# Kernel tuning notes

Hardware: AMD Instinct MI355X
Metric: run time of the kernel (lower is better)

Reference implementation:

```python
import jax, jax.numpy as jnp
import numpy as np

V, E, H, L = 32000, 512, 512, 2   # vocab, emb_dim, hidden_dim, lstm layers
IN = 2 * H                        # input_size (= enc_output feature dim)
B, S_ENC, T_DEC = 32, 128, 64


def setup_inputs() -> dict:
    key = jax.random.key(0)
    ks = jax.random.split(key, 20)
    sc = 0.05
    inp = {
        "tokens": jax.random.randint(ks[0], (B, T_DEC), 0, V),
        "enc_output": jax.random.normal(ks[1], (B, S_ENC, IN), jnp.float32),
        "enc_h": jax.random.normal(ks[2], (L, B, H), jnp.float32),
        "enc_c": jax.random.normal(ks[3], (L, B, H), jnp.float32),
        "emb": jax.random.normal(ks[4], (V, E), jnp.float32) * sc,
        # attention MLP: attn1 in = H*L + IN, out = 4H; attn2: 4H -> 1
        "attn1_w": jax.random.normal(ks[5], (4 * H, H * L + IN), jnp.float32) * sc,
        "attn1_b": jnp.zeros((4 * H,), jnp.float32),
        "attn2_w": jax.random.normal(ks[6], (1, 4 * H), jnp.float32) * sc,
        "attn2_b": jnp.zeros((1,), jnp.float32),
        # LSTM layer 0: input E + IN; layer 1: input H. PyTorch gate order i,f,g,o
        "w_ih0": jax.random.normal(ks[7], (4 * H, E + IN), jnp.float32) * sc,
        "w_hh0": jax.random.normal(ks[8], (4 * H, H), jnp.float32) * sc,
        "b_ih0": jnp.zeros((4 * H,), jnp.float32),
        "b_hh0": jnp.zeros((4 * H,), jnp.float32),
        "w_ih1": jax.random.normal(ks[9], (4 * H, H), jnp.float32) * sc,
        "w_hh1": jax.random.normal(ks[10], (4 * H, H), jnp.float32) * sc,
        "b_ih1": jnp.zeros((4 * H,), jnp.float32),
        "b_hh1": jnp.zeros((4 * H,), jnp.float32),
        "out_w": jax.random.normal(ks[11], (V, H), jnp.float32) * sc,
        "out_b": jnp.zeros((V,), jnp.float32),
    }
    return inp


def _lstm_cell(x, h, c, w_ih, w_hh, b_ih, b_hh):
    g = x @ w_ih.T + h @ w_hh.T + (b_ih + b_hh)
    i, f, gg, o = jnp.split(g, 4, axis=-1)
    c_new = jax.nn.sigmoid(f) * c + jax.nn.sigmoid(i) * jnp.tanh(gg)
    h_new = jax.nn.sigmoid(o) * jnp.tanh(c_new)
    return h_new, c_new


def reference(tokens, enc_output, enc_h, enc_c, emb,
              attn1_w, attn1_b, attn2_w, attn2_b,
              w_ih0, w_hh0, b_ih0, b_hh0,
              w_ih1, w_hh1, b_ih1, b_hh1,
              out_w, out_b):
    b, s_enc = enc_output.shape[0], enc_output.shape[1]

    def context(h):  # h: [L, B, H] -> context: [B, 2H]
        hflat = jnp.transpose(h, (1, 0, 2)).reshape(b, -1)          # [B, L*H]
        hexp = jnp.broadcast_to(hflat[:, None, :], (b, s_enc, hflat.shape[-1]))
        ai = jnp.concatenate([enc_output, hexp], axis=-1)           # [B, S, 2H+L*H]
        hid = ai @ attn1_w.T + attn1_b                               # [B, S, 4H]
        logits = hid @ attn2_w.T + attn2_b                           # [B, S, 1]
        w = jax.nn.softmax(logits, axis=1)
        return jnp.sum(enc_output * w, axis=1)                       # [B, 2H]

    def step(carry, emb_t):  # emb_t: [B, E]
        h, c = carry
        ctx = context(h)
        x = jnp.concatenate([emb_t, ctx], axis=-1)                   # [B, E+2H]
        h0, c0 = _lstm_cell(x, h[0], c[0], w_ih0, w_hh0, b_ih0, b_hh0)
        h1, c1 = _lstm_cell(h0, h[1], c[1], w_ih1, w_hh1, b_ih1, b_hh1)
        return (jnp.stack([h0, h1]), jnp.stack([c0, c1])), h1

    emb_seq = jnp.transpose(emb[tokens], (1, 0, 2))                  # [T, B, E]
    _, outs = jax.lax.scan(step, (enc_h, enc_c), emb_seq)            # [T, B, H]
    dec = jnp.transpose(outs, (1, 0, 2))                             # [B, T, H]
    return dec @ out_w.T + out_b                                     # [B, T, V]
```

## Files before the change

kernel.cpp:

```cpp
#include <hip/hip_runtime.h>
#include <hip/hip_bf16.h>

typedef __attribute__((ext_vector_type(4))) float f4v;
typedef __attribute__((ext_vector_type(4))) short s4v;
typedef __attribute__((ext_vector_type(8))) short s8v;

#define DEVINL __device__ __forceinline__
#define NBLK 128
#define PADK 536
#define WROWS (16 * PADK)
#define HSLOT 16384

DEVINL short f2bf(float f) {
  unsigned u = __float_as_uint(f);
  u += 0x7FFFu + ((u >> 16) & 1u);
  return (short)(u >> 16);
}
DEVINL float bf2f(short s) {
  return __uint_as_float(((unsigned)(unsigned short)s) << 16);
}
DEVINL float sigm(float x) { return 1.f / (1.f + expf(-x)); }

DEVINL void cstore64(short* p, unsigned long long d) {
  asm volatile("global_store_dwordx2 %0, %1, off sc0 sc1"
               :: "v"(p), "v"(d) : "memory");
}

__global__ __launch_bounds__(256) void k_init2(const float* __restrict__ enc_h,
                                               short* __restrict__ hbuf,
                                               unsigned* __restrict__ arr) {
  int i = blockIdx.x * 256 + threadIdx.x;
  hbuf[i] = f2bf(enc_h[i]);
  hbuf[(long)65 * HSLOT + i] = f2bf(enc_h[16384 + i]);
  if (i < NBLK * 32 + 32) arr[i] = ((i & 31) == 16) ? 1u : 0u;
}

__global__ __launch_bounds__(256) void k_weff(const float* __restrict__ attn1_w,
                                              const float* __restrict__ attn2_w,
                                              float* __restrict__ w_enc) {
  __shared__ float part[8][32];
  int t = threadIdx.x;
  int jl = t & 31, kp = t >> 5;
  int j = blockIdx.x * 32 + jl;
  float acc = 0.f;
  for (int k = kp * 256; k < kp * 256 + 256; ++k)
    acc += attn2_w[k] * attn1_w[(long)k * 2048 + j];
  part[kp][jl] = acc;
  __syncthreads();
  if (t < 32) {
    float s = 0.f;
    for (int p = 0; p < 8; ++p) s += part[p][t];
    w_enc[blockIdx.x * 32 + t] = s;
  }
}

__global__ __launch_bounds__(256) void k_attn(const float* __restrict__ enc,
                                              const float* __restrict__ w_enc,
                                              float* __restrict__ ctx) {
  __shared__ float red[256];
  __shared__ float wls[128];
  int b = blockIdx.x, t = threadIdx.x;
  int s = t >> 1, half = t & 1;
  const float* e = enc + ((long)b * 128 + s) * 1024 + half * 512;
  const float* wv = w_enc + half * 512;
  float acc = 0.f;
  for (int k = 0; k < 512; k += 4) {
    f4v ev = *(const f4v*)(e + k);
    f4v w4 = *(const f4v*)(wv + k);
    acc += ev[0] * w4[0] + ev[1] * w4[1] + ev[2] * w4[2] + ev[3] * w4[3];
  }
  red[t] = acc;
  __syncthreads();
  if (half == 0) wls[s] = red[t] + red[t + 1];
  __syncthreads();
  red[t] = (t < 128) ? wls[t] : -3.4e38f;
  __syncthreads();
  for (int off = 128; off >= 1; off >>= 1) {
    if (t < off) red[t] = fmaxf(red[t], red[t + off]);
    __syncthreads();
  }
  float mx = red[0];
  __syncthreads();
  if (t < 128) { float ex = expf(wls[t] - mx); wls[t] = ex; red[t] = ex; }
  else red[t] = 0.f;
  __syncthreads();
  for (int off = 128; off >= 1; off >>= 1) {
    if (t < off) red[t] += red[t + off];
    __syncthreads();
  }
  float inv = 1.f / red[0];
  __syncthreads();
  if (t < 128) wls[t] *= inv;
  __syncthreads();
  float a0 = 0.f, a1 = 0.f, a2 = 0.f, a3 = 0.f;
  for (int ss = 0; ss < 128; ++ss) {
    float w = wls[ss];
    const float* er = enc + ((long)b * 128 + ss) * 1024;
    a0 += w * er[t];
    a1 += w * er[t + 256];
    a2 += w * er[t + 512];
    a3 += w * er[t + 768];
  }
  ctx[b * 1024 + t] = a0;
  ctx[b * 1024 + t + 256] = a1;
  ctx[b * 1024 + t + 512] = a2;
  ctx[b * 1024 + t + 768] = a3;
}

__global__ __launch_bounds__(256) void k_ctxpre(const float* __restrict__ w_ih0,
                                                const float* __restrict__ b_ih0,
                                                const float* __restrict__ b_hh0,
                                                const float* __restrict__ ctx,
                                                float* __restrict__ ctxpre) {
  int t = threadIdx.x;
  int j = blockIdx.x * 8 + (t >> 5);
  int b = t & 31;
  float acc = b_ih0[j] + b_hh0[j];
  const float* w = w_ih0 + (long)j * 1536 + 512;
  const float* c = ctx + b * 1024;
  for (int k = 0; k < 1024; k += 4) {
    f4v wv = *(const f4v*)(w + k);
    f4v cv = *(const f4v*)(c + k);
    acc += wv[0] * cv[0] + wv[1] * cv[1] + wv[2] * cv[2] + wv[3] * cv[3];
  }
  ctxpre[b * 2048 + j] = acc;
}

__global__ __launch_bounds__(256) void k_cvt(const float* __restrict__ src,
                                             short* __restrict__ dst) {
  long i = ((long)blockIdx.x * 256 + threadIdx.x) * 8;
  f4v a = *(const f4v*)(src + i);
  f4v b = *(const f4v*)(src + i + 4);
  s8v o;
  o[0] = f2bf(a[0]); o[1] = f2bf(a[1]); o[2] = f2bf(a[2]); o[3] = f2bf(a[3]);
  o[4] = f2bf(b[0]); o[5] = f2bf(b[1]); o[6] = f2bf(b[2]); o[7] = f2bf(b[3]);
  *(s8v*)(dst + i) = o;
}

template <int MODE>
__global__ __launch_bounds__(256) void gemm_bf16(
    const float* __restrict__ A, const float* __restrict__ B,
    const int* __restrict__ a_rows, const float* __restrict__ bias,
    float* __restrict__ C, int K, int lda, int ldb, int ldc) {
  __shared__ short As[128 * 72];
  __shared__ short Bs[128 * 72];
  int n0 = blockIdx.x * 128, m0 = blockIdx.y * 128;
  int t = threadIdx.x;
  int lane = t & 63, w = t >> 6;
  int wm = w & 1, wn = w >> 1;
  f4v acc[4][4];
#pragma unroll
  for (int mi = 0; mi < 4; ++mi)
#pragma unroll
    for (int ni = 0; ni < 4; ++ni) acc[mi][ni] = (f4v){0.f, 0.f, 0.f, 0.f};

  int sr = t >> 1;
  int sh = (t & 1) * 32;
  long arow = a_rows ? (long)a_rows[m0 + sr] : (long)(m0 + sr);
  const float* ap = A + arow * lda + sh;
  const float* bp = B + (long)(n0 + sr) * ldb + sh;
  short* as = &As[sr * 72 + sh];
  short* bs = &Bs[sr * 72 + sh];

  for (int k0 = 0; k0 < K; k0 += 64) {
#pragma unroll
    for (int i = 0; i < 8; ++i) {
      f4v va = *(const f4v*)(ap + k0 + i * 4);
      f4v vb = *(const f4v*)(bp + k0 + i * 4);
      s4v sa, sb;
      sa[0] = f2bf(va[0]); sa[1] = f2bf(va[1]); sa[2] = f2bf(va[2]); sa[3] = f2bf(va[3]);
      sb[0] = f2bf(vb[0]); sb[1] = f2bf(vb[1]); sb[2] = f2bf(vb[2]); sb[3] = f2bf(vb[3]);
      *(s4v*)(as + i * 4) = sa;
      *(s4v*)(bs + i * 4) = sb;
    }
    __syncthreads();
#pragma unroll
    for (int ks = 0; ks < 2; ++ks) {
      s8v af[4], bf[4];
#pragma unroll
      for (int mi = 0; mi < 4; ++mi)
        af[mi] = *(const s8v*)&As[(wm * 64 + mi * 16 + (lane & 15)) * 72 + ks * 32 + (lane >> 4) * 8];
#pragma unroll
      for (int ni = 0; ni < 4; ++ni)
        bf[ni] = *(const s8v*)&Bs[(wn * 64 + ni * 16 + (lane & 15)) * 72 + ks * 32 + (lane >> 4) * 8];
#pragma unroll
      for (int mi = 0; mi < 4; ++mi)
#pragma unroll
        for (int ni = 0; ni < 4; ++ni)
          acc[mi][ni] = __builtin_amdgcn_mfma_f32_16x16x32_bf16(af[mi], bf[ni], acc[mi][ni], 0, 0, 0);
    }
    __syncthreads();
  }
  int fq = lane >> 4, fr = lane & 15;
#pragma unroll
  for (int mi = 0; mi < 4; ++mi)
#pragma unroll
    for (int ni = 0; ni < 4; ++ni) {
      int col = n0 + wn * 64 + ni * 16 + fr;
      long rowb = m0 + wm * 64 + mi * 16 + fq * 4;
      if (MODE == 2) {
        int bz = (col & 511) >> 2;
        int c = ((col >> 9) << 2) + (col & 3);
#pragma unroll
        for (int r = 0; r < 4; ++r) {
          long m = rowb + r;
          C[(long)bz * 32768 + (m & 63) * 512 + (m >> 6) * 16 + c] = acc[mi][ni][r];
        }
      } else {
        float bv = bias ? bias[col] : 0.f;
#pragma unroll
        for (int r = 0; r < 4; ++r) C[(rowb + r) * (long)ldc + col] = acc[mi][ni][r] + bv;
      }
    }
}

template <bool BCVT>
__global__ __launch_bounds__(256) void gemm_out(
    const short* __restrict__ A, const short* __restrict__ Bbf,
    const float* __restrict__ Bf, const float* __restrict__ bias,
    float* __restrict__ C) {
  __shared__ short As[128 * 72];
  __shared__ short Bs[128 * 72];
  int m0 = blockIdx.x * 128, n0 = blockIdx.y * 128;
  int t = threadIdx.x;
  int lane = t & 63, w = t >> 6;
  int wm = w & 1, wn = w >> 1;
  f4v acc[4][4];
#pragma unroll
  for (int mi = 0; mi < 4; ++mi)
#pragma unroll
    for (int ni = 0; ni < 4; ++ni) acc[mi][ni] = (f4v){0.f, 0.f, 0.f, 0.f};

  int sr = t >> 1;
  int sh = (t & 1) * 32;
  const short* ap = A + (long)(m0 + sr) * 512 + sh;
  const short* bpb = Bbf + (long)(n0 + sr) * 512 + sh;
  const float* bpf = Bf + (long)(n0 + sr) * 512 + sh;
  short* as = &As[sr * 72 + sh];
  short* bs = &Bs[sr * 72 + sh];

  for (int k0 = 0; k0 < 512; k0 += 64) {
#pragma unroll
    for (int i = 0; i < 4; ++i)
      *(s8v*)(as + i * 8) = *(const s8v*)(ap + k0 + i * 8);
    if (BCVT) {
#pragma unroll
      for (int i = 0; i < 8; ++i) {
        f4v vb = *(const f4v*)(bpf + k0 + i * 4);
        s4v sb;
        sb[0] = f2bf(vb[0]); sb[1] = f2bf(vb[1]); sb[2] = f2bf(vb[2]); sb[3] = f2bf(vb[3]);
        *(s4v*)(bs + i * 4) = sb;
      }
    } else {
#pragma unroll
      for (int i = 0; i < 4; ++i)
        *(s8v*)(bs + i * 8) = *(const s8v*)(bpb + k0 + i * 8);
    }
    __syncthreads();
#pragma unroll
    for (int ks = 0; ks < 2; ++ks) {
      s8v af[4], bf[4];
#pragma unroll
      for (int mi = 0; mi < 4; ++mi)
        af[mi] = *(const s8v*)&As[(wm * 64 + mi * 16 + (lane & 15)) * 72 + ks * 32 + (lane >> 4) * 8];
#pragma unroll
      for (int ni = 0; ni < 4; ++ni)
        bf[ni] = *(const s8v*)&Bs[(wn * 64 + ni * 16 + (lane & 15)) * 72 + ks * 32 + (lane >> 4) * 8];
#pragma unroll
      for (int mi = 0; mi < 4; ++mi)
#pragma unroll
        for (int ni = 0; ni < 4; ++ni)
          acc[mi][ni] = __builtin_amdgcn_mfma_f32_16x16x32_bf16(af[mi], bf[ni], acc[mi][ni], 0, 0, 0);
    }
    __syncthreads();
  }
  int fq = lane >> 4, fr = lane & 15;
#pragma unroll
  for (int mi = 0; mi < 4; ++mi)
#pragma unroll
    for (int ni = 0; ni < 4; ++ni) {
      int col = n0 + wn * 64 + ni * 16 + fr;
      float bv = bias[col];
      long rowb = m0 + wm * 64 + mi * 16 + fq * 4;
#pragma unroll
      for (int r = 0; r < 4; ++r)
        __builtin_nontemporal_store(acc[mi][ni][r] + bv, &C[(rowb + r) * 32000L + col]);
    }
}

__global__ __launch_bounds__(256, 1) void lstm_persist(
    const float* __restrict__ w_hh0, const float* __restrict__ w_ih1,
    const float* __restrict__ w_hh1,
    const float* __restrict__ b_ih1, const float* __restrict__ b_hh1,
    const float* __restrict__ enc_c,
    const float* __restrict__ embp2, const float* __restrict__ ctxpre,
    short* __restrict__ hbuf, short* __restrict__ h1seqbf,
    unsigned* __restrict__ arr) {
  __shared__ alignas(16) short wlds[6 * WROWS];
  __shared__ float ctxp_l[32][16];
  __shared__ float bias1_l[16];
  __shared__ float gbuf[2][2][32][17];

  const int tid = threadIdx.x;
  const int hb4 = blockIdx.x * 4;
  const int lane = tid & 63, wid = tid >> 6;
  const int mt = wid & 1, kh = wid >> 1;
  const int fr = lane & 15, fq = lane >> 4;

  for (int base = tid * 4; base < 48 * 512; base += 1024) {
    int row = base >> 9, k = base & 511;
    int m = row >> 4, c = row & 15;
    int j = ((c >> 2) << 9) + hb4 + (c & 3);
    const float* wsrc = (m == 0) ? w_hh0 : ((m == 1) ? w_ih1 : w_hh1);
    f4v v = *(const f4v*)(wsrc + (long)j * 512 + k);
    short* hi = &wlds[(m * 2) * WROWS + c * PADK + k];
    short* lo = &wlds[(m * 2 + 1) * WROWS + c * PADK + k];
#pragma unroll
    for (int e = 0; e < 4; ++e) {
      short hh = f2bf(v[e]);
      hi[e] = hh;
      lo[e] = f2bf(v[e] - bf2f(hh));
    }
  }
  for (int i = tid; i < 512; i += 256) {
    int b = i >> 4, c = i & 15;
    ctxp_l[b][c] = ctxpre[b * 2048 + ((c >> 2) << 9) + hb4 + (c & 3)];
  }
  if (tid < 16) {
    int j = ((tid >> 2) << 9) + hb4 + (tid & 3);
    bias1_l[tid] = b_ih1[j] + b_hh1[j];
  }
  const int cq = (tid & 127) >> 2, cr = tid & 3;
  float c0r = 0.f, c1r = 0.f;
  if (tid < 128) c0r = enc_c[cq * 512 + hb4 + cr];
  else           c1r = enc_c[16384 + cq * 512 + hb4 + cr];
  __syncthreads();
  asm volatile("s_waitcnt vmcnt(0)" ::: "memory");
  asm volatile("buffer_inv sc1" ::: "memory");
  __syncthreads();

  short* H0 = hbuf;
  short* H1 = hbuf + (long)65 * HSLOT;
  const int foff = (mt * 16 + fr) * 512 + kh * 256 + fq * 8;
  const int woff = fr * PADK + kh * 256 + fq * 8;

  for (int p = 0; p <= 64; ++p) {
    const bool do_l0 = (p < 64), do_l1 = (p > 0);
    float e4[4] = {0.f, 0.f, 0.f, 0.f};
    if (do_l0 && tid < 128) {
      const float* ep = embp2 + (long)blockIdx.x * 32768 + p * 512 + cq * 16 + cr;
#pragma unroll
      for (int g = 0; g < 4; ++g) e4[g] = ep[g * 4];
    }
    if (p) {
      if (tid < NBLK)
        while (__hip_atomic_load(&arr[tid << 5], __ATOMIC_RELAXED,
                                 __HIP_MEMORY_SCOPE_AGENT) < (unsigned)p)
          __builtin_amdgcn_s_sleep(1);
      __syncthreads();
    }
    const short* a0 = H0 + (long)p * HSLOT + foff;
    s8v A0[8];
#pragma unroll
    for (int ks = 0; ks < 8; ++ks) A0[ks] = *(const s8v*)(a0 + ks * 32);
    if (do_l0) {
      f4v l0h = {0.f, 0.f, 0.f, 0.f}, l0l = l0h;
      const short* b0h = &wlds[0 * WROWS + woff];
      const short* b0l = &wlds[1 * WROWS + woff];
#pragma unroll
      for (int ks = 0; ks < 8; ++ks) {
        s8v B0h = *(const s8v*)(b0h + ks * 32);
        s8v B0l = *(const s8v*)(b0l + ks * 32);
        l0h = __builtin_amdgcn_mfma_f32_16x16x32_bf16(A0[ks], B0h, l0h, 0, 0, 0);
        l0l = __builtin_amdgcn_mfma_f32_16x16x32_bf16(A0[ks], B0l, l0l, 0, 0, 0);
      }
      f4v s = l0h + l0l;
#pragma unroll
      for (int r = 0; r < 4; ++r) gbuf[0][kh][mt * 16 + fq * 4 + r][fr] = s[r];
    }
    __syncthreads();
    if (do_l0) {
      if (tid < 128) {
        float g4[4];
#pragma unroll
        for (int g = 0; g < 4; ++g) {
          int c = g * 4 + cr;
          g4[g] = gbuf[0][0][cq][c] + gbuf[0][1][cq][c] + ctxp_l[cq][c] + e4[g];
        }
        float cn = sigm(g4[1]) * c0r + sigm(g4[0]) * tanhf(g4[2]);
        float hn = sigm(g4[3]) * tanhf(cn);
        c0r = cn;
        unsigned v16 = (unsigned)(unsigned short)f2bf(hn);
        unsigned p01 = v16 | ((unsigned)__shfl_down((int)v16, 1) << 16);
        unsigned long long wd = (unsigned long long)p01 |
            ((unsigned long long)(unsigned)__shfl_down((int)p01, 2) << 32);
        if ((tid & 3) == 0)
          cstore64(H0 + (long)(p + 1) * HSLOT + cq * 512 + hb4, wd);
      }
      asm volatile("s_waitcnt vmcnt(0)" ::: "memory");
      __syncthreads();
      if (tid == 0)
        __hip_atomic_store(&arr[(unsigned)blockIdx.x << 5], (unsigned)(p + 1),
                           __ATOMIC_RELAXED, __HIP_MEMORY_SCOPE_AGENT);
    }
    if (do_l1) {
      f4v x1h = {0.f, 0.f, 0.f, 0.f}, x1l = x1h, h1h = x1h, h1l = x1h;
      const short* b2h = &wlds[2 * WROWS + woff];
      const short* b2l = &wlds[3 * WROWS + woff];
#pragma unroll
      for (int ks = 0; ks < 8; ++ks) {
        s8v B2h = *(const s8v*)(b2h + ks * 32);
        s8v B2l = *(const s8v*)(b2l + ks * 32);
        x1h = __builtin_amdgcn_mfma_f32_16x16x32_bf16(A0[ks], B2h, x1h, 0, 0, 0);
        x1l = __builtin_amdgcn_mfma_f32_16x16x32_bf16(A0[ks], B2l, x1l, 0, 0, 0);
      }
      if (tid < NBLK)
        while (__hip_atomic_load(&arr[(tid << 5) + 16], __ATOMIC_RELAXED,
                                 __HIP_MEMORY_SCOPE_AGENT) < (unsigned)p)
          __builtin_amdgcn_s_sleep(1);
      __syncthreads();
      const short* a1 = H1 + (long)(p - 1) * HSLOT + foff;
      const short* b4h = &wlds[4 * WROWS + woff];
      const short* b4l = &wlds[5 * WROWS + woff];
#pragma unroll
      for (int ks = 0; ks < 8; ++ks) {
        s8v A1 = *(const s8v*)(a1 + ks * 32);
        s8v B4h = *(const s8v*)(b4h + ks * 32);
        s8v B4l = *(const s8v*)(b4l + ks * 32);
        h1h = __builtin_amdgcn_mfma_f32_16x16x32_bf16(A1, B4h, h1h, 0, 0, 0);
        h1l = __builtin_amdgcn_mfma_f32_16x16x32_bf16(A1, B4l, h1l, 0, 0, 0);
      }
      f4v s = x1h + x1l + h1h + h1l;
#pragma unroll
      for (int r = 0; r < 4; ++r) gbuf[1][kh][mt * 16 + fq * 4 + r][fr] = s[r];
      __syncthreads();
      if (tid >= 128) {
        float g4[4];
#pragma unroll
        for (int g = 0; g < 4; ++g) {
          int c = g * 4 + cr;
          g4[g] = gbuf[1][0][cq][c] + gbuf[1][1][cq][c] + bias1_l[c];
        }
        float cn = sigm(g4[1]) * c1r + sigm(g4[0]) * tanhf(g4[2]);
        float hn = sigm(g4[3]) * tanhf(cn);
        c1r = cn;
        unsigned v16 = (unsigned)(unsigned short)f2bf(hn);
        unsigned p01 = v16 | ((unsigned)__shfl_down((int)v16, 1) << 16);
        unsigned long long wd = (unsigned long long)p01 |
            ((unsigned long long)(unsigned)__shfl_down((int)p01, 2) << 32);
        if ((tid & 3) == 0) {
          if (p < 64)
            cstore64(H1 + (long)p * HSLOT + cq * 512 + hb4, wd);
          *(unsigned long long*)&h1seqbf[((long)cq * 64 + (p - 1)) * 512 + hb4] = wd;
        }
      }
      if (p < 64) {
        asm volatile("s_waitcnt vmcnt(0)" ::: "memory");
        __syncthreads();
        if (tid == 0)
          __hip_atomic_store(&arr[((unsigned)blockIdx.x << 5) + 16],
                             (unsigned)(p + 1), __ATOMIC_RELAXED,
                             __HIP_MEMORY_SCOPE_AGENT);
      }
    }
  }
}

extern "C" void kernel_launch(void* const* d_in, const int* in_sizes, int n_in,
                              void* d_out, int out_size, void* d_ws, size_t ws_size,
                              hipStream_t stream) {
  const int*   tokens  = (const int*)  d_in[0];
  const float* enc_out = (const float*)d_in[1];
  const float* enc_h   = (const float*)d_in[2];
  const float* enc_c   = (const float*)d_in[3];
  const float* emb     = (const float*)d_in[4];
  const float* attn1_w = (const float*)d_in[5];
  const float* attn2_w = (const float*)d_in[7];
  const float* w_ih0   = (const float*)d_in[9];
  const float* w_hh0   = (const float*)d_in[10];
  const float* b_ih0   = (const float*)d_in[11];
  const float* b_hh0   = (const float*)d_in[12];
  const float* w_ih1   = (const float*)d_in[13];
  const float* w_hh1   = (const float*)d_in[14];
  const float* b_ih1   = (const float*)d_in[15];
  const float* b_hh1   = (const float*)d_in[16];
  const float* out_w   = (const float*)d_in[17];
  const float* out_b   = (const float*)d_in[18];
  float* out = (float*)d_out;

  float* f = (float*)d_ws;
  float*    w_enc    = f;
  float*    ctx      = f + 1024;
  float*    ctxpre   = f + 33792;
  float*    embp2    = f + 99328;
  short*    h1seqbf  = (short*)(f + 4293632);
  short*    hbuf     = (short*)(f + 4817920);
  unsigned* arr      = (unsigned*)(f + 5882880);
  short*    out_w_bf = (short*)(f + 5887040);
  const size_t NEED = (size_t)(5887040 + 8192000) * 4;
  const bool big = ws_size >= NEED;

  k_init2<<<64, 256, 0, stream>>>(enc_h, hbuf, arr);
  k_weff<<<32, 256, 0, stream>>>(attn1_w, attn2_w, w_enc);
  k_attn<<<32, 256, 0, stream>>>(enc_out, w_enc, ctx);
  k_ctxpre<<<256, 256, 0, stream>>>(w_ih0, b_ih0, b_hh0, ctx, ctxpre);
  gemm_bf16<2><<<dim3(16, 16), 256, 0, stream>>>(emb, w_ih0, tokens, nullptr,
                                                 embp2, 512, 512, 1536, 0);
  if (big) k_cvt<<<8000, 256, 0, stream>>>(out_w, out_w_bf);
  lstm_persist<<<NBLK, 256, 0, stream>>>(w_hh0, w_ih1, w_hh1, b_ih1, b_hh1, enc_c,
                                         embp2, ctxpre, hbuf, h1seqbf, arr);
  if (big)
    gemm_out<false><<<dim3(16, 250), 256, 0, stream>>>(h1seqbf, out_w_bf, nullptr,
                                                       out_b, out);
  else
    gemm_out<true><<<dim3(16, 250), 256, 0, stream>>>(h1seqbf, nullptr, out_w,
                                                      out_b, out);
}
```

Before: 644.9 us.

## Split persistent LSTM into separate layer-0 and layer-1 block groups

```diff
diff --git a/kernel.cpp b/kernel.cpp
--- a/kernel.cpp
+++ b/kernel.cpp
@@ -32,7 +32,7 @@
   int i = blockIdx.x * 256 + threadIdx.x;
   hbuf[i] = f2bf(enc_h[i]);
   hbuf[(long)65 * HSLOT + i] = f2bf(enc_h[16384 + i]);
-  if (i < NBLK * 32 + 32) arr[i] = ((i & 31) == 16) ? 1u : 0u;
+  if (i < NBLK * 32 + 32) arr[i] = 0u;
 }
 
 __global__ __launch_bounds__(256) void k_weff(const float* __restrict__ attn1_w,
@@ -299,19 +299,22 @@
   __shared__ alignas(16) short wlds[6 * WROWS];
   __shared__ float ctxp_l[32][16];
   __shared__ float bias1_l[16];
-  __shared__ float gbuf[2][2][32][17];
+  __shared__ float gbuf[2][32][17];
 
   const int tid = threadIdx.x;
-  const int hb4 = blockIdx.x * 4;
+  const bool is_l0 = (blockIdx.x < NBLK);
+  const int bz = is_l0 ? blockIdx.x : blockIdx.x - NBLK;
+  const int hb4 = bz * 4;
   const int lane = tid & 63, wid = tid >> 6;
   const int mt = wid & 1, kh = wid >> 1;
   const int fr = lane & 15, fq = lane >> 4;
 
-  for (int base = tid * 4; base < 48 * 512; base += 1024) {
+  const int nmat = is_l0 ? 1 : 2;
+  for (int base = tid * 4; base < nmat * 16 * 512; base += 1024) {
     int row = base >> 9, k = base & 511;
     int m = row >> 4, c = row & 15;
     int j = ((c >> 2) << 9) + hb4 + (c & 3);
-    const float* wsrc = (m == 0) ? w_hh0 : ((m == 1) ? w_ih1 : w_hh1);
+    const float* wsrc = is_l0 ? w_hh0 : (m == 0 ? w_ih1 : w_hh1);
     f4v v = *(const f4v*)(wsrc + (long)j * 512 + k);
     short* hi = &wlds[(m * 2) * WROWS + c * PADK + k];
     short* lo = &wlds[(m * 2 + 1) * WROWS + c * PADK + k];
@@ -322,18 +325,19 @@
       lo[e] = f2bf(v[e] - bf2f(hh));
     }
   }
-  for (int i = tid; i < 512; i += 256) {
-    int b = i >> 4, c = i & 15;
-    ctxp_l[b][c] = ctxpre[b * 2048 + ((c >> 2) << 9) + hb4 + (c & 3)];
-  }
-  if (tid < 16) {
+  if (is_l0) {
+    for (int i = tid; i < 512; i += 256) {
+      int b = i >> 4, c = i & 15;
+      ctxp_l[b][c] = ctxpre[b * 2048 + ((c >> 2) << 9) + hb4 + (c & 3)];
+    }
+  } else if (tid < 16) {
     int j = ((tid >> 2) << 9) + hb4 + (tid & 3);
     bias1_l[tid] = b_ih1[j] + b_hh1[j];
   }
   const int cq = (tid & 127) >> 2, cr = tid & 3;
-  float c0r = 0.f, c1r = 0.f;
-  if (tid < 128) c0r = enc_c[cq * 512 + hb4 + cr];
-  else           c1r = enc_c[16384 + cq * 512 + hb4 + cr];
+  float cst = 0.f;
+  if (tid < 128)
+    cst = enc_c[(is_l0 ? 0 : 16384) + cq * 512 + hb4 + cr];
   __syncthreads();
   asm volatile("s_waitcnt vmcnt(0)" ::: "memory");
   asm volatile("buffer_inv sc1" ::: "memory");
@@ -344,52 +348,47 @@
   const int foff = (mt * 16 + fr) * 512 + kh * 256 + fq * 8;
   const int woff = fr * PADK + kh * 256 + fq * 8;
 
-  for (int p = 0; p <= 64; ++p) {
-    const bool do_l0 = (p < 64), do_l1 = (p > 0);
-    float e4[4] = {0.f, 0.f, 0.f, 0.f};
-    if (do_l0 && tid < 128) {
-      const float* ep = embp2 + (long)blockIdx.x * 32768 + p * 512 + cq * 16 + cr;
-#pragma unroll
-      for (int g = 0; g < 4; ++g) e4[g] = ep[g * 4];
-    }
-    if (p) {
-      if (tid < NBLK)
-        while (__hip_atomic_load(&arr[tid << 5], __ATOMIC_RELAXED,
-                                 __HIP_MEMORY_SCOPE_AGENT) < (unsigned)p)
-          __builtin_amdgcn_s_sleep(1);
-      __syncthreads();
-    }
-    const short* a0 = H0 + (long)p * HSLOT + foff;
-    s8v A0[8];
-#pragma unroll
-    for (int ks = 0; ks < 8; ++ks) A0[ks] = *(const s8v*)(a0 + ks * 32);
-    if (do_l0) {
+  if (is_l0) {
+    for (int p = 0; p < 64; ++p) {
+      float e4[4];
+      if (tid < 128) {
+        const float* ep = embp2 + (long)bz * 32768 + p * 512 + cq * 16 + cr;
+#pragma unroll
+        for (int g = 0; g < 4; ++g) e4[g] = ep[g * 4];
+      }
+      if (p) {
+        if (tid < NBLK)
+          while (__hip_atomic_load(&arr[tid << 5], __ATOMIC_RELAXED,
+                                   __HIP_MEMORY_SCOPE_AGENT) < (unsigned)p)
+            __builtin_amdgcn_s_sleep(1);
+        __syncthreads();
+      }
+      const short* a0 = H0 + (long)p * HSLOT + foff;
       f4v l0h = {0.f, 0.f, 0.f, 0.f}, l0l = l0h;
       const short* b0h = &wlds[0 * WROWS + woff];
       const short* b0l = &wlds[1 * WROWS + woff];
 #pragma unroll
       for (int ks = 0; ks < 8; ++ks) {
+        s8v A0 = *(const s8v*)(a0 + ks * 32);
         s8v B0h = *(const s8v*)(b0h + ks * 32);
         s8v B0l = *(const s8v*)(b0l + ks * 32);
-        l0h = __builtin_amdgcn_mfma_f32_16x16x32_bf16(A0[ks], B0h, l0h, 0, 0, 0);
-        l0l = __builtin_amdgcn_mfma_f32_16x16x32_bf16(A0[ks], B0l, l0l, 0, 0, 0);
+        l0h = __builtin_amdgcn_mfma_f32_16x16x32_bf16(A0, B0h, l0h, 0, 0, 0);
+        l0l = __builtin_amdgcn_mfma_f32_16x16x32_bf16(A0, B0l, l0l, 0, 0, 0);
       }
       f4v s = l0h + l0l;
 #pragma unroll
-      for (int r = 0; r < 4; ++r) gbuf[0][kh][mt * 16 + fq * 4 + r][fr] = s[r];
-    }
-    __syncthreads();
-    if (do_l0) {
+      for (int r = 0; r < 4; ++r) gbuf[kh][mt * 16 + fq * 4 + r][fr] = s[r];
+      __syncthreads();
       if (tid < 128) {
         float g4[4];
 #pragma unroll
         for (int g = 0; g < 4; ++g) {
           int c = g * 4 + cr;
-          g4[g] = gbuf[0][0][cq][c] + gbuf[0][1][cq][c] + ctxp_l[cq][c] + e4[g];
+          g4[g] = gbuf[0][cq][c] + gbuf[1][cq][c] + ctxp_l[cq][c] + e4[g];
         }
-        float cn = sigm(g4[1]) * c0r + sigm(g4[0]) * tanhf(g4[2]);
+        float cn = sigm(g4[1]) * cst + sigm(g4[0]) * tanhf(g4[2]);
         float hn = sigm(g4[3]) * tanhf(cn);
-        c0r = cn;
+        cst = cn;
         unsigned v16 = (unsigned)(unsigned short)f2bf(hn);
         unsigned p01 = v16 | ((unsigned)__shfl_down((int)v16, 1) << 16);
         unsigned long long wd = (unsigned long long)p01 |
@@ -400,28 +399,38 @@
       asm volatile("s_waitcnt vmcnt(0)" ::: "memory");
       __syncthreads();
       if (tid == 0)
-        __hip_atomic_store(&arr[(unsigned)blockIdx.x << 5], (unsigned)(p + 1),
+        __hip_atomic_store(&arr[(unsigned)bz << 5], (unsigned)(p + 1),
                            __ATOMIC_RELAXED, __HIP_MEMORY_SCOPE_AGENT);
     }
-    if (do_l1) {
+  } else {
+    for (int p = 1; p <= 64; ++p) {
+      if (tid < NBLK)
+        while (__hip_atomic_load(&arr[tid << 5], __ATOMIC_RELAXED,
+                                 __HIP_MEMORY_SCOPE_AGENT) < (unsigned)p)
+          __builtin_amdgcn_s_sleep(2);
+      __syncthreads();
+      const short* a0 = H0 + (long)p * HSLOT + foff;
       f4v x1h = {0.f, 0.f, 0.f, 0.f}, x1l = x1h, h1h = x1h, h1l = x1h;
-      const short* b2h = &wlds[2 * WROWS + woff];
-      const short* b2l = &wlds[3 * WROWS + woff];
+      const short* b2h = &wlds[0 * WROWS + woff];
+      const short* b2l = &wlds[1 * WROWS + woff];
 #pragma unroll
       for (int ks = 0; ks < 8; ++ks) {
+        s8v A0 = *(const s8v*)(a0 + ks * 32);
         s8v B2h = *(const s8v*)(b2h + ks * 32);
         s8v B2l = *(const s8v*)(b2l + ks * 32);
-        x1h = __builtin_amdgcn_mfma_f32_16x16x32_bf16(A0[ks], B2h, x1h, 0, 0, 0);
-        x1l = __builtin_amdgcn_mfma_f32_16x16x32_bf16(A0[ks], B2l, x1l, 0, 0, 0);
-      }
-      if (tid < NBLK)
-        while (__hip_atomic_load(&arr[(tid << 5) + 16], __ATOMIC_RELAXED,
-                                 __HIP_MEMORY_SCOPE_AGENT) < (unsigned)p)
-          __builtin_amdgcn_s_sleep(1);
-      __syncthreads();
+        x1h = __builtin_amdgcn_mfma_f32_16x16x32_bf16(A0, B2h, x1h, 0, 0, 0);
+        x1l = __builtin_amdgcn_mfma_f32_16x16x32_bf16(A0, B2l, x1l, 0, 0, 0);
+      }
+      if (p > 1) {
+        if (tid < NBLK)
+          while (__hip_atomic_load(&arr[(tid << 5) + 16], __ATOMIC_RELAXED,
+                                   __HIP_MEMORY_SCOPE_AGENT) < (unsigned)(p - 1))
+            __builtin_amdgcn_s_sleep(2);
+        __syncthreads();
+      }
       const short* a1 = H1 + (long)(p - 1) * HSLOT + foff;
-      const short* b4h = &wlds[4 * WROWS + woff];
-      const short* b4l = &wlds[5 * WROWS + woff];
+      const short* b4h = &wlds[2 * WROWS + woff];
+      const short* b4l = &wlds[3 * WROWS + woff];
 #pragma unroll
       for (int ks = 0; ks < 8; ++ks) {
         s8v A1 = *(const s8v*)(a1 + ks * 32);
@@ -432,18 +441,18 @@
       }
       f4v s = x1h + x1l + h1h + h1l;
 #pragma unroll
-      for (int r = 0; r < 4; ++r) gbuf[1][kh][mt * 16 + fq * 4 + r][fr] = s[r];
+      for (int r = 0; r < 4; ++r) gbuf[kh][mt * 16 + fq * 4 + r][fr] = s[r];
       __syncthreads();
-      if (tid >= 128) {
+      if (tid < 128) {
         float g4[4];
 #pragma unroll
         for (int g = 0; g < 4; ++g) {
           int c = g * 4 + cr;
-          g4[g] = gbuf[1][0][cq][c] + gbuf[1][1][cq][c] + bias1_l[c];
+          g4[g] = gbuf[0][cq][c] + gbuf[1][cq][c] + bias1_l[c];
         }
-        float cn = sigm(g4[1]) * c1r + sigm(g4[0]) * tanhf(g4[2]);
+        float cn = sigm(g4[1]) * cst + sigm(g4[0]) * tanhf(g4[2]);
         float hn = sigm(g4[3]) * tanhf(cn);
-        c1r = cn;
+        cst = cn;
         unsigned v16 = (unsigned)(unsigned short)f2bf(hn);
         unsigned p01 = v16 | ((unsigned)__shfl_down((int)v16, 1) << 16);
         unsigned long long wd = (unsigned long long)p01 |
@@ -458,9 +467,8 @@
         asm volatile("s_waitcnt vmcnt(0)" ::: "memory");
         __syncthreads();
         if (tid == 0)
-          __hip_atomic_store(&arr[((unsigned)blockIdx.x << 5) + 16],
-                             (unsigned)(p + 1), __ATOMIC_RELAXED,
-                             __HIP_MEMORY_SCOPE_AGENT);
+          __hip_atomic_store(&arr[((unsigned)bz << 5) + 16], (unsigned)p,
+                             __ATOMIC_RELAXED, __HIP_MEMORY_SCOPE_AGENT);
       }
     }
   }
@@ -507,8 +515,9 @@
   gemm_bf16<2><<<dim3(16, 16), 256, 0, stream>>>(emb, w_ih0, tokens, nullptr,
                                                  embp2, 512, 512, 1536, 0);
   if (big) k_cvt<<<8000, 256, 0, stream>>>(out_w, out_w_bf);
-  lstm_persist<<<NBLK, 256, 0, stream>>>(w_hh0, w_ih1, w_hh1, b_ih1, b_hh1, enc_c,
-                                         embp2, ctxpre, hbuf, h1seqbf, arr);
+  lstm_persist<<<2 * NBLK, 256, 0, stream>>>(w_hh0, w_ih1, w_hh1, b_ih1, b_hh1,
+                                             enc_c, embp2, ctxpre, hbuf,
+                                             h1seqbf, arr);
   if (big)
     gemm_out<false><<<dim3(16, 250), 256, 0, stream>>>(h1seqbf, out_w_bf, nullptr,
                                                        out_b, out);
```

Measured after the change: 556.1 us. 13.8% less time.
